# Kernel tuning notes

Measured on AMD Instinct MI355X. Metric: run time of the kernel, lower is better.

Reference implementation:

```python
import jax, jax.numpy as jnp
import numpy as np

EPS = 1e-6

def _layernorm(x, g, b):
    m = jnp.mean(x, axis=-1, keepdims=True)
    v = jnp.var(x, axis=-1, keepdims=True)
    return (x - m) / jnp.sqrt(v + EPS) * g + b

def setup_inputs() -> dict:
    key = jax.random.key(0)
    ks = jax.random.split(key, 12)
    B, L, D, H = 2, 1024, 1024, 16
    s = 0.02  # weight init scale
    return {
        "query": jax.random.normal(ks[0], (B, L, D), jnp.float32),
        "pos_bias": jax.random.normal(ks[1], (H, L, L), jnp.float32) * 0.1,
        "postag_bias": jax.random.normal(ks[2], (B, H, L, L), jnp.float32) * 0.1,
        "lex_mask": jax.random.normal(ks[3], (B, L), jnp.float32) * 0.1,
        "mask": jax.random.randint(ks[4], (B, L), 0, 2).astype(jnp.int32),
        "Wq": jax.random.normal(ks[5], (D, D), jnp.float32) * s,
        "bq": jnp.zeros((D,), jnp.float32),
        "Wk": jax.random.normal(ks[6], (D, D), jnp.float32) * s,
        "bk": jnp.zeros((D,), jnp.float32),
        "Wv": jax.random.normal(ks[7], (D, D), jnp.float32) * s,
        "bv": jnp.zeros((D,), jnp.float32),
        "Wo": jax.random.normal(ks[8], (D, D), jnp.float32) * s,
        "bo": jnp.zeros((D,), jnp.float32),
        "gamma": jnp.ones((D,), jnp.float32),
        "beta": jnp.zeros((D,), jnp.float32),
    }

def reference(query, pos_bias, postag_bias, lex_mask, mask,
              Wq, bq, Wk, bk, Wv, bv, Wo, bo, gamma, beta):
    B, L, D = query.shape
    H = pos_bias.shape[0]
    dk = D // H
    scale = jnp.asarray(dk ** 0.5, query.dtype)

    residual = query
    context = query              # context=None path: set BEFORE pre-LN norm
    qn = _layernorm(query, gamma, beta)  # pre_ln=True applies only to query

    Q = (qn @ Wq.T + bq).reshape(B, L, H, dk)       # bqhd
    K = (context @ Wk.T + bk).reshape(B, L, H, dk)  # bkhd
    V = (context @ Wv.T + bv).reshape(B, L, H, dk)

    # (B,H,L,S) logits with all additive bias terms
    logits = jnp.einsum('bqhd,bkhd->bhqk', Q, K) / scale
    logits = logits + pos_bias[None]               # rel-pos bias (H,L,S)
    logits = logits + postag_bias                  # POS-tag bias (B,H,L,S)
    logits = logits + lex_mask[:, None, None, :]   # additive lexical mask
    logits = jnp.where(mask[:, None, None, :] == 0, -jnp.inf, logits)

    attn = jax.nn.softmax(logits, axis=-1)         # dropout inactive (eval)
    out = jnp.einsum('bhqk,bkhd->bqhd', attn, V).reshape(B, L, D)
    out = out @ Wo.T + bo
    out = out + residual
    return out, attn
```

## Files before the change

kernel.cpp:

```cpp
#include <hip/hip_runtime.h>
#include <hip/hip_bf16.h>
#include <math.h>

constexpr int B = 2, L = 1024, D = 1024, H = 16, DK = 64;
constexpr int M = B * L;
constexpr int DD = D * D;

typedef __attribute__((ext_vector_type(8))) short bf16x8;
typedef __attribute__((ext_vector_type(4))) float f32x4;

__device__ inline unsigned short f2bf(float f) {
    __hip_bfloat16 h = __float2bfloat16(f);
    return __builtin_bit_cast(unsigned short, h);
}

__device__ inline void glds16(const void* g, void* l) {
    __builtin_amdgcn_global_load_lds((const __attribute__((address_space(1))) void*)g,
                                     (__attribute__((address_space(3))) void*)l,
                                     16, 0, 0);
}

__global__ __launch_bounds__(256) void ln2_kernel(const float* __restrict__ x,
                                                  const float* __restrict__ gamma,
                                                  const float* __restrict__ beta,
                                                  const float* __restrict__ lex,
                                                  const int* __restrict__ mask,
                                                  unsigned short* __restrict__ qn16,
                                                  unsigned short* __restrict__ q16,
                                                  float* __restrict__ lsmout) {
    int row = blockIdx.x;
    int t = threadIdx.x;
    if (t == 0) lsmout[row] = mask[row] ? lex[row] : -1e30f;
    const float4 v = ((const float4*)(x + (size_t)row * D))[t];
    float s  = v.x + v.y + v.z + v.w;
    float sq = v.x*v.x + v.y*v.y + v.z*v.z + v.w*v.w;
    #pragma unroll
    for (int m = 32; m >= 1; m >>= 1) {
        s  += __shfl_xor(s, m, 64);
        sq += __shfl_xor(sq, m, 64);
    }
    __shared__ float rs[4], rq[4];
    int wid = t >> 6;
    if ((t & 63) == 0) { rs[wid] = s; rq[wid] = sq; }
    __syncthreads();
    s  = rs[0] + rs[1] + rs[2] + rs[3];
    sq = rq[0] + rq[1] + rq[2] + rq[3];
    float mean = s * (1.0f / D);
    float var  = sq * (1.0f / D) - mean * mean;
    float rstd = rsqrtf(var + 1e-6f);
    float4 g  = ((const float4*)gamma)[t];
    float4 bb = ((const float4*)beta)[t];
    ushort4 on, oq;
    on.x = f2bf((v.x - mean) * rstd * g.x + bb.x);
    on.y = f2bf((v.y - mean) * rstd * g.y + bb.y);
    on.z = f2bf((v.z - mean) * rstd * g.z + bb.z);
    on.w = f2bf((v.w - mean) * rstd * g.w + bb.w);
    oq.x = f2bf(v.x); oq.y = f2bf(v.y); oq.z = f2bf(v.z); oq.w = f2bf(v.w);
    ((ushort4*)(qn16 + (size_t)row * D))[t] = on;
    ((ushort4*)(q16  + (size_t)row * D))[t] = oq;
}

__global__ __launch_bounds__(256) void wconv_kernel(const float* __restrict__ Wq,
                                                    const float* __restrict__ Wk,
                                                    const float* __restrict__ Wv,
                                                    const float* __restrict__ Wo,
                                                    unsigned short* __restrict__ out) {
    const float* src = (blockIdx.y == 0) ? Wq : (blockIdx.y == 1) ? Wk
                       : (blockIdx.y == 2) ? Wv : Wo;
    size_t i = (size_t)blockIdx.x * 256 + threadIdx.x;
    float4 v = ((const float4*)src)[i];
    ushort4 o;
    o.x = f2bf(v.x); o.y = f2bf(v.y); o.z = f2bf(v.z); o.w = f2bf(v.w);
    ((ushort4*)(out + (size_t)blockIdx.y * DD))[i] = o;
}

__global__ __launch_bounds__(256) void gemm_qkv(
        const unsigned short* __restrict__ qn16, const unsigned short* __restrict__ q16,
        const unsigned short* __restrict__ W,
        const float* __restrict__ bq, const float* __restrict__ bk,
        const float* __restrict__ bv,
        unsigned short* __restrict__ Qm, unsigned short* __restrict__ Km,
        unsigned short* __restrict__ Vm) {
    __shared__ __align__(16) unsigned short As[128 * 64];
    __shared__ __align__(16) unsigned short Ws[128 * 64];
    int t = threadIdx.x, lane = t & 63, w = t >> 6;
    int quad = lane >> 4, l15 = lane & 15;
    int nt = blockIdx.x;
    int bm = blockIdx.y * 128;
    const unsigned short* A = (nt < 8) ? qn16 : q16;
    const float* bias = (nt < 8) ? bq : ((nt < 16) ? bk : bv);
    unsigned short* Cout = (nt < 8) ? Qm : ((nt < 16) ? Km : Vm);
    int bn_local = (nt & 7) * 128;
    int wm = (w >> 1) * 64, wn = (w & 1) * 64;
    f32x4 acc[4][4] = {};
    for (int k0 = 0; k0 < D; k0 += 64) {
        __syncthreads();
        const unsigned short* ap = A + (size_t)(bm + w * 32) * D + k0;
        const unsigned short* wp = W + (size_t)(nt * 128 + w * 32) * D + k0;
        #pragma unroll
        for (int i = 0; i < 4; i++) {
            int c = i * 64 + lane;
            int r = c >> 3, g = (c & 7) ^ (r & 7);
            glds16(ap + (size_t)r * D + g * 8, &As[w * 2048 + i * 512]);
            glds16(wp + (size_t)r * D + g * 8, &Ws[w * 2048 + i * 512]);
        }
        __syncthreads();
        #pragma unroll
        for (int k2 = 0; k2 < 2; k2++) {
            bf16x8 av[4], bw[4];
            #pragma unroll
            for (int i = 0; i < 4; i++) {
                int r = wm + i * 16 + l15;
                av[i] = *(const bf16x8*)&As[r * 64 + (((quad + 4 * k2) ^ (r & 7)) * 8)];
            }
            #pragma unroll
            for (int j = 0; j < 4; j++) {
                int r = wn + j * 16 + l15;
                bw[j] = *(const bf16x8*)&Ws[r * 64 + (((quad + 4 * k2) ^ (r & 7)) * 8)];
            }
            #pragma unroll
            for (int i = 0; i < 4; i++)
                #pragma unroll
                for (int j = 0; j < 4; j++)
                    acc[i][j] = __builtin_amdgcn_mfma_f32_16x16x32_bf16(av[i], bw[j], acc[i][j], 0, 0, 0);
        }
    }
    #pragma unroll
    for (int j = 0; j < 4; j++) {
        int col = bn_local + wn + j * 16 + l15;
        float bcol = bias[col];
        #pragma unroll
        for (int i = 0; i < 4; i++)
            #pragma unroll
            for (int rg = 0; rg < 4; rg++) {
                int row = bm + wm + i * 16 + quad * 4 + rg;
                Cout[(size_t)row * D + col] = f2bf(acc[i][j][rg] + bcol);
            }
    }
}

__global__ __launch_bounds__(256) void vtrans_kernel(const unsigned short* __restrict__ Vm,
                                                     unsigned short* __restrict__ Vt) {
    __shared__ unsigned short sb[128 * 66];
    int t = threadIdx.x;
    int z = blockIdx.y;
    int b = z >> 4, h = z & 15;
    int s0 = blockIdx.x * 128;
    size_t base = (size_t)b * L * D + (size_t)h * 64;
    #pragma unroll
    for (int i = 0; i < 4; i++) {
        int idx = t + 256 * i;
        int r = idx >> 3, c8 = idx & 7;
        uint4 vv = *(const uint4*)&Vm[base + (size_t)(s0 + r) * D + c8 * 8];
        unsigned int* sp = (unsigned int*)&sb[r * 66 + c8 * 8];
        sp[0] = vv.x; sp[1] = vv.y; sp[2] = vv.z; sp[3] = vv.w;
    }
    __syncthreads();
    #pragma unroll
    for (int i = 0; i < 4; i++) {
        int idx = t + 256 * i;
        int d = idx >> 4, sc = idx & 15;
        unsigned short tmp[8];
        #pragma unroll
        for (int j = 0; j < 8; j++) tmp[j] = sb[(sc * 8 + j) * 66 + d];
        *(uint4*)&Vt[((size_t)z * 64 + d) * L + s0 + sc * 8] = *(uint4*)tmp;
    }
}

__global__ __launch_bounds__(256, 3) void attn_pv_kernel(
        const unsigned short* __restrict__ Qm, const unsigned short* __restrict__ Km,
        const unsigned short* __restrict__ Vt,
        const float* __restrict__ pos_bias, const float* __restrict__ postag,
        const float* __restrict__ lsm, float* __restrict__ attn_out,
        unsigned short* __restrict__ ctx16) {
    __shared__ __align__(16) unsigned short q_sh[16][72];
    __shared__ __align__(16) unsigned short p_sh[2][16][136];
    __shared__ float lsm_sh[1024];
    __shared__ float redA[16][4], redB[16][4];

    int t = threadIdx.x, lane = t & 63, w = t >> 6;
    int quad = lane >> 4, l15 = lane & 15;
    int qt = blockIdx.x & 63;
    int bh = blockIdx.x >> 6;
    int b = bh >> 4, h = bh & 15;
    int q0 = qt * 16;
    int q = q0 + l15;
    size_t base = (size_t)b * L * D + (size_t)h * DK;

    if (t < 128) {
        int r = t >> 3, c8 = t & 7;
        *(uint4*)&q_sh[r][c8 * 8] = *(const uint4*)&Qm[base + (size_t)(q0 + r) * D + c8 * 8];
    }
    ((float4*)lsm_sh)[t] = ((const float4*)(lsm + b * L))[t];
    __syncthreads();
    bf16x8 qb0 = *(const bf16x8*)&q_sh[l15][quad * 8];
    bf16x8 qb1 = *(const bf16x8*)&q_sh[l15][32 + quad * 8];

    const float* pbp = pos_bias + ((size_t)h * L + q) * L;
    const float* ptp = postag + ((size_t)bh * L + q) * L;
    const unsigned short* kp0 = Km + base + (size_t)((w) * 16 + l15) * D + quad * 8;
    const unsigned short* kp1 = Km + base + (size_t)((4 + w) * 16 + l15) * D + quad * 8;

    f32x4 acc[16] = {};
    #pragma unroll
    for (int st = 0; st < 8; st++) {
        size_t ko = (size_t)st * 128 * D;
        bf16x8 ka00 = *(const bf16x8*)(kp0 + ko);
        bf16x8 ka01 = *(const bf16x8*)(kp0 + ko + 32);
        bf16x8 ka10 = *(const bf16x8*)(kp1 + ko);
        bf16x8 ka11 = *(const bf16x8*)(kp1 + ko + 32);
        int s_u0 = st * 128 + w * 16 + quad * 4;
        int s_u1 = s_u0 + 64;
        float4 pb0 = *(const float4*)(pbp + s_u0);
        float4 pt0 = *(const float4*)(ptp + s_u0);
        float4 pb1 = *(const float4*)(pbp + s_u1);
        float4 pt1 = *(const float4*)(ptp + s_u1);
        float4 l0 = *(const float4*)&lsm_sh[s_u0];
        float4 l1 = *(const float4*)&lsm_sh[s_u1];
        int ti0 = 2 * st, ti1 = 2 * st + 1;
        acc[ti0] = __builtin_amdgcn_mfma_f32_16x16x32_bf16(ka00, qb0, acc[ti0], 0, 0, 0);
        acc[ti0] = __builtin_amdgcn_mfma_f32_16x16x32_bf16(ka01, qb1, acc[ti0], 0, 0, 0);
        acc[ti1] = __builtin_amdgcn_mfma_f32_16x16x32_bf16(ka10, qb0, acc[ti1], 0, 0, 0);
        acc[ti1] = __builtin_amdgcn_mfma_f32_16x16x32_bf16(ka11, qb1, acc[ti1], 0, 0, 0);
        acc[ti0][0] = acc[ti0][0] * 0.125f + (pb0.x + pt0.x + l0.x);
        acc[ti0][1] = acc[ti0][1] * 0.125f + (pb0.y + pt0.y + l0.y);
        acc[ti0][2] = acc[ti0][2] * 0.125f + (pb0.z + pt0.z + l0.z);
        acc[ti0][3] = acc[ti0][3] * 0.125f + (pb0.w + pt0.w + l0.w);
        acc[ti1][0] = acc[ti1][0] * 0.125f + (pb1.x + pt1.x + l1.x);
        acc[ti1][1] = acc[ti1][1] * 0.125f + (pb1.y + pt1.y + l1.y);
        acc[ti1][2] = acc[ti1][2] * 0.125f + (pb1.z + pt1.z + l1.z);
        acc[ti1][3] = acc[ti1][3] * 0.125f + (pb1.w + pt1.w + l1.w);
    }
    float mx = -1e30f;
    #pragma unroll
    for (int ti = 0; ti < 16; ti++)
        #pragma unroll
        for (int rg = 0; rg < 4; rg++) mx = fmaxf(mx, acc[ti][rg]);
    mx = fmaxf(mx, __shfl_xor(mx, 16, 64));
    mx = fmaxf(mx, __shfl_xor(mx, 32, 64));
    if (quad == 0) redA[l15][w] = mx;
    __syncthreads();
    mx = fmaxf(fmaxf(redA[l15][0], redA[l15][1]), fmaxf(redA[l15][2], redA[l15][3]));
    float sum = 0.f;
    #pragma unroll
    for (int ti = 0; ti < 16; ti++)
        #pragma unroll
        for (int rg = 0; rg < 4; rg++) {
            float e = __expf(acc[ti][rg] - mx);
            acc[ti][rg] = e;
            sum += e;
        }
    sum += __shfl_xor(sum, 16, 64);
    sum += __shfl_xor(sum, 32, 64);
    if (quad == 0) redB[l15][w] = sum;
    __syncthreads();
    float inv = 1.0f / (redB[l15][0] + redB[l15][1] + redB[l15][2] + redB[l15][3]);
    #pragma unroll
    for (int ti = 0; ti < 16; ti++) {
        int s0 = (ti >> 1) * 128 + (ti & 1) * 64 + w * 16 + quad * 4;
        float4 o;
        o.x = acc[ti][0] * inv; o.y = acc[ti][1] * inv;
        o.z = acc[ti][2] * inv; o.w = acc[ti][3] * inv;
        acc[ti][0] = o.x; acc[ti][1] = o.y; acc[ti][2] = o.z; acc[ti][3] = o.w;
        *(float4*)&attn_out[((size_t)bh * L + q) * L + s0] = o;
    }
    const unsigned short* vpl = Vt + ((size_t)bh * 64 + w * 16 + l15) * L + quad * 8;
    f32x4 cacc = {};
    bf16x8 vcur[4];
    #pragma unroll
    for (int kk = 0; kk < 4; kk++)
        vcur[kk] = *(const bf16x8*)(vpl + kk * 32);
    #pragma unroll
    for (int st = 0; st < 8; st++) {
        #pragma unroll
        for (int u = 0; u < 2; u++) {
            f32x4 p = acc[2 * st + u];
            ushort4 pu;
            pu.x = f2bf(p[0]); pu.y = f2bf(p[1]); pu.z = f2bf(p[2]); pu.w = f2bf(p[3]);
            *(ushort4*)&p_sh[st & 1][l15][u * 64 + w * 16 + quad * 4] = pu;
        }
        bf16x8 vnext[4];
        if (st < 7) {
            #pragma unroll
            for (int kk = 0; kk < 4; kk++)
                vnext[kk] = *(const bf16x8*)(vpl + (st + 1) * 128 + kk * 32);
        }
        asm volatile("s_waitcnt lgkmcnt(0)" ::: "memory");
        __builtin_amdgcn_sched_barrier(0);
        __builtin_amdgcn_s_barrier();
        __builtin_amdgcn_sched_barrier(0);
        #pragma unroll
        for (int kk = 0; kk < 4; kk++) {
            bf16x8 pf = *(const bf16x8*)&p_sh[st & 1][l15][kk * 32 + quad * 8];
            cacc = __builtin_amdgcn_mfma_f32_16x16x32_bf16(pf, vcur[kk], cacc, 0, 0, 0);
        }
        if (st < 7) {
            #pragma unroll
            for (int kk = 0; kk < 4; kk++) vcur[kk] = vnext[kk];
        }
    }
    size_t cbase = ((size_t)b * L + q0) * D + (size_t)h * 64 + w * 16 + l15;
    #pragma unroll
    for (int rg = 0; rg < 4; rg++)
        ctx16[cbase + (size_t)(quad * 4 + rg) * D] = f2bf(cacc[rg]);
}

__global__ __launch_bounds__(256) void gemm_out(
        const unsigned short* __restrict__ A, const unsigned short* __restrict__ W,
        const float* __restrict__ bias, const float* __restrict__ res,
        float* __restrict__ C) {
    __shared__ __align__(16) unsigned short As[64 * 64];
    __shared__ __align__(16) unsigned short Ws[64 * 64];
    int t = threadIdx.x, lane = t & 63, w = t >> 6;
    int quad = lane >> 4, l15 = lane & 15;
    int bm = blockIdx.x * 64, bn = blockIdx.y * 64;
    int wm = (w >> 1) * 32, wn = (w & 1) * 32;
    f32x4 acc[2][2] = {};
    for (int k0 = 0; k0 < D; k0 += 64) {
        __syncthreads();
        const unsigned short* ap = A + (size_t)(bm + w * 16) * D + k0;
        const unsigned short* wp = W + (size_t)(bn + w * 16) * D + k0;
        #pragma unroll
        for (int i = 0; i < 2; i++) {
            int c = i * 64 + lane;
            int r = c >> 3, g = (c & 7) ^ (r & 7);
            glds16(ap + (size_t)r * D + g * 8, &As[w * 1024 + i * 512]);
            glds16(wp + (size_t)r * D + g * 8, &Ws[w * 1024 + i * 512]);
        }
        __syncthreads();
        #pragma unroll
        for (int k2 = 0; k2 < 2; k2++) {
            bf16x8 av[2], bw[2];
            #pragma unroll
            for (int i = 0; i < 2; i++) {
                int r = wm + i * 16 + l15;
                av[i] = *(const bf16x8*)&As[r * 64 + (((quad + 4 * k2) ^ (r & 7)) * 8)];
            }
            #pragma unroll
            for (int j = 0; j < 2; j++) {
                int r = wn + j * 16 + l15;
                bw[j] = *(const bf16x8*)&Ws[r * 64 + (((quad + 4 * k2) ^ (r & 7)) * 8)];
            }
            #pragma unroll
            for (int i = 0; i < 2; i++)
                #pragma unroll
                for (int j = 0; j < 2; j++)
                    acc[i][j] = __builtin_amdgcn_mfma_f32_16x16x32_bf16(av[i], bw[j], acc[i][j], 0, 0, 0);
        }
    }
    #pragma unroll
    for (int j = 0; j < 2; j++) {
        int col = bn + wn + j * 16 + l15;
        float bcol = bias[col];
        #pragma unroll
        for (int i = 0; i < 2; i++)
            #pragma unroll
            for (int rg = 0; rg < 4; rg++) {
                int row = bm + wm + i * 16 + quad * 4 + rg;
                C[(size_t)row * D + col] = acc[i][j][rg] + bcol + res[(size_t)row * D + col];
            }
    }
}

extern "C" void kernel_launch(void* const* d_in, const int* in_sizes, int n_in,
                              void* d_out, int out_size, void* d_ws, size_t ws_size,
                              hipStream_t stream) {
    (void)in_sizes; (void)n_in; (void)out_size; (void)ws_size;
    const float* query  = (const float*)d_in[0];
    const float* pos_b  = (const float*)d_in[1];
    const float* postag = (const float*)d_in[2];
    const float* lex    = (const float*)d_in[3];
    const int*   mask   = (const int*)d_in[4];
    const float* Wq = (const float*)d_in[5];
    const float* bq = (const float*)d_in[6];
    const float* Wk = (const float*)d_in[7];
    const float* bk = (const float*)d_in[8];
    const float* Wv = (const float*)d_in[9];
    const float* bv = (const float*)d_in[10];
    const float* Wo = (const float*)d_in[11];
    const float* bo = (const float*)d_in[12];
    const float* gamma = (const float*)d_in[13];
    const float* beta  = (const float*)d_in[14];

    float* out  = (float*)d_out;
    float* attn = out + (size_t)B * L * D;

    unsigned short* ws16 = (unsigned short*)d_ws;
    const size_t NE = (size_t)M * D;
    unsigned short* qn16  = ws16;
    unsigned short* q16   = ws16 + NE;
    unsigned short* W16   = ws16 + 2 * NE;
    unsigned short* Qm16  = W16 + 4 * (size_t)DD;
    unsigned short* Km16  = Qm16 + NE;
    unsigned short* Vm16  = Km16 + NE;
    unsigned short* Vt16  = Vm16 + NE;
    unsigned short* ctx16 = Vt16 + NE;
    float* lsm = (float*)(ctx16 + NE);

    ln2_kernel<<<M, 256, 0, stream>>>(query, gamma, beta, lex, mask, qn16, q16, lsm);
    wconv_kernel<<<dim3(DD / 1024, 4), 256, 0, stream>>>(Wq, Wk, Wv, Wo, W16);
    gemm_qkv<<<dim3(24, 16), 256, 0, stream>>>(qn16, q16, W16, bq, bk, bv,
                                               Qm16, Km16, Vm16);
    vtrans_kernel<<<dim3(8, 32), 256, 0, stream>>>(Vm16, Vt16);
    attn_pv_kernel<<<B * H * (L / 16), 256, 0, stream>>>(Qm16, Km16, Vt16,
                                                         pos_b, postag, lsm,
                                                         attn, ctx16);
    gemm_out<<<dim3(32, 16), 256, 0, stream>>>(ctx16, W16 + 3 * (size_t)DD, bo, query, out);
}
```

Baseline: 432.1 us.

## Stage K, bias and V tiles through swizzled LDS with async global_load_lds double-buffering

```diff
diff --git a/kernel.cpp b/kernel.cpp
--- a/kernel.cpp
+++ b/kernel.cpp
@@ -8,6 +8,8 @@
 
 typedef __attribute__((ext_vector_type(8))) short bf16x8;
 typedef __attribute__((ext_vector_type(4))) float f32x4;
+
+#define SB0() __builtin_amdgcn_sched_barrier(0)
 
 __device__ inline unsigned short f2bf(float f) {
     __hip_bfloat16 h = __float2bfloat16(f);
@@ -167,14 +169,15 @@
     }
 }
 
-__global__ __launch_bounds__(256, 3) void attn_pv_kernel(
+__global__ __launch_bounds__(256, 2) void attn_pv_kernel(
         const unsigned short* __restrict__ Qm, const unsigned short* __restrict__ Km,
         const unsigned short* __restrict__ Vt,
         const float* __restrict__ pos_bias, const float* __restrict__ postag,
         const float* __restrict__ lsm, float* __restrict__ attn_out,
         unsigned short* __restrict__ ctx16) {
+    __shared__ __align__(16) unsigned short pool[32768];
+    __shared__ __align__(16) unsigned short p_sh[16][136];
     __shared__ __align__(16) unsigned short q_sh[16][72];
-    __shared__ __align__(16) unsigned short p_sh[2][16][136];
     __shared__ float lsm_sh[1024];
     __shared__ float redA[16][4], redB[16][4];
 
@@ -196,28 +199,80 @@
     bf16x8 qb0 = *(const bf16x8*)&q_sh[l15][quad * 8];
     bf16x8 qb1 = *(const bf16x8*)&q_sh[l15][32 + quad * 8];
 
-    const float* pbp = pos_bias + ((size_t)h * L + q) * L;
-    const float* ptp = postag + ((size_t)bh * L + q) * L;
-    const unsigned short* kp0 = Km + base + (size_t)((w) * 16 + l15) * D + quad * 8;
-    const unsigned short* kp1 = Km + base + (size_t)((4 + w) * 16 + l15) * D + quad * 8;
+    const float* pbQ = pos_bias + ((size_t)h * L + q0) * L;
+    const float* ptQ = postag + ((size_t)bh * L + q0) * L;
 
     f32x4 acc[16] = {};
+    SB0();
+    {
+        const unsigned short* kpn = Km + base + (size_t)(w * 32) * D;
+        #pragma unroll
+        for (int i = 0; i < 4; i++) {
+            int r = i * 8 + (lane >> 3);
+            int g = (lane & 7) ^ (r & 7);
+            glds16(kpn + (size_t)r * D + g * 8, &pool[w * 2048 + i * 512]);
+        }
+    }
+    SB0();
+    {
+        int rb = lane >> 3;
+        int gb = (lane & 7) ^ rb;
+        #pragma unroll
+        for (int i = 0; i < 2; i++) {
+            glds16(pbQ + (size_t)(i * 8 + rb) * L + w * 32 + gb * 4,
+                   &pool[16384 + w * 2048 + i * 512]);
+            glds16(ptQ + (size_t)(i * 8 + rb) * L + w * 32 + gb * 4,
+                   &pool[16384 + w * 2048 + 1024 + i * 512]);
+        }
+    }
+    SB0();
     #pragma unroll
     for (int st = 0; st < 8; st++) {
-        size_t ko = (size_t)st * 128 * D;
-        bf16x8 ka00 = *(const bf16x8*)(kp0 + ko);
-        bf16x8 ka01 = *(const bf16x8*)(kp0 + ko + 32);
-        bf16x8 ka10 = *(const bf16x8*)(kp1 + ko);
-        bf16x8 ka11 = *(const bf16x8*)(kp1 + ko + 32);
-        int s_u0 = st * 128 + w * 16 + quad * 4;
-        int s_u1 = s_u0 + 64;
-        float4 pb0 = *(const float4*)(pbp + s_u0);
-        float4 pt0 = *(const float4*)(ptp + s_u0);
-        float4 pb1 = *(const float4*)(pbp + s_u1);
-        float4 pt1 = *(const float4*)(ptp + s_u1);
+        int bc = st & 1, bn = bc ^ 1;
+        if (st < 7) {
+            SB0();
+            const unsigned short* kpn = Km + base + (size_t)((st + 1) * 128 + w * 32) * D;
+            #pragma unroll
+            for (int i = 0; i < 4; i++) {
+                int r = i * 8 + (lane >> 3);
+                int g = (lane & 7) ^ (r & 7);
+                glds16(kpn + (size_t)r * D + g * 8, &pool[bn * 8192 + w * 2048 + i * 512]);
+            }
+            SB0();
+            {
+                int rb = lane >> 3;
+                int gb = (lane & 7) ^ rb;
+                #pragma unroll
+                for (int i = 0; i < 2; i++) {
+                    glds16(pbQ + (size_t)(i * 8 + rb) * L + (st + 1) * 128 + w * 32 + gb * 4,
+                           &pool[16384 + bn * 8192 + w * 2048 + i * 512]);
+                    glds16(ptQ + (size_t)(i * 8 + rb) * L + (st + 1) * 128 + w * 32 + gb * 4,
+                           &pool[16384 + bn * 8192 + w * 2048 + 1024 + i * 512]);
+                }
+            }
+            SB0();
+            asm volatile("s_waitcnt vmcnt(8)" ::: "memory");
+        } else {
+            SB0();
+            asm volatile("s_waitcnt vmcnt(0)" ::: "memory");
+        }
+        SB0();
+        int r7 = l15 & 7;
+        const unsigned short* kB = &pool[bc * 8192 + w * 2048];
+        bf16x8 ka00 = *(const bf16x8*)&kB[l15 * 64 + ((quad ^ r7) * 8)];
+        bf16x8 ka01 = *(const bf16x8*)&kB[l15 * 64 + (((quad + 4) ^ r7) * 8)];
+        bf16x8 ka10 = *(const bf16x8*)&kB[(16 + l15) * 64 + ((quad ^ r7) * 8)];
+        bf16x8 ka11 = *(const bf16x8*)&kB[(16 + l15) * 64 + (((quad + 4) ^ r7) * 8)];
+        const float* pbL = (const float*)&pool[16384 + bc * 8192 + w * 2048];
+        const float* ptL = (const float*)&pool[16384 + bc * 8192 + w * 2048 + 1024];
+        float4 pb0 = *(const float4*)&pbL[l15 * 32 + ((quad ^ r7) * 4)];
+        float4 pb1 = *(const float4*)&pbL[l15 * 32 + (((quad + 4) ^ r7) * 4)];
+        float4 pt0 = *(const float4*)&ptL[l15 * 32 + ((quad ^ r7) * 4)];
+        float4 pt1 = *(const float4*)&ptL[l15 * 32 + (((quad + 4) ^ r7) * 4)];
+        int s_u0 = st * 128 + w * 32 + quad * 4;
         float4 l0 = *(const float4*)&lsm_sh[s_u0];
-        float4 l1 = *(const float4*)&lsm_sh[s_u1];
-        int ti0 = 2 * st, ti1 = 2 * st + 1;
+        float4 l1 = *(const float4*)&lsm_sh[s_u0 + 16];
+        int ti0 = 2 * st, ti1 = ti0 + 1;
         acc[ti0] = __builtin_amdgcn_mfma_f32_16x16x32_bf16(ka00, qb0, acc[ti0], 0, 0, 0);
         acc[ti0] = __builtin_amdgcn_mfma_f32_16x16x32_bf16(ka01, qb1, acc[ti0], 0, 0, 0);
         acc[ti1] = __builtin_amdgcn_mfma_f32_16x16x32_bf16(ka10, qb0, acc[ti1], 0, 0, 0);
@@ -257,47 +312,62 @@
     float inv = 1.0f / (redB[l15][0] + redB[l15][1] + redB[l15][2] + redB[l15][3]);
     #pragma unroll
     for (int ti = 0; ti < 16; ti++) {
-        int s0 = (ti >> 1) * 128 + (ti & 1) * 64 + w * 16 + quad * 4;
+        int s0 = (ti >> 1) * 128 + w * 32 + (ti & 1) * 16 + quad * 4;
         float4 o;
         o.x = acc[ti][0] * inv; o.y = acc[ti][1] * inv;
         o.z = acc[ti][2] * inv; o.w = acc[ti][3] * inv;
         acc[ti][0] = o.x; acc[ti][1] = o.y; acc[ti][2] = o.z; acc[ti][3] = o.w;
         *(float4*)&attn_out[((size_t)bh * L + q) * L + s0] = o;
     }
-    const unsigned short* vpl = Vt + ((size_t)bh * 64 + w * 16 + l15) * L + quad * 8;
     f32x4 cacc = {};
-    bf16x8 vcur[4];
-    #pragma unroll
-    for (int kk = 0; kk < 4; kk++)
-        vcur[kk] = *(const bf16x8*)(vpl + kk * 32);
+    const unsigned short* vbase = Vt + ((size_t)bh * 64 + w * 16) * L;
+    SB0();
+    #pragma unroll
+    for (int i = 0; i < 4; i++) {
+        int r = i * 4 + (lane >> 4);
+        int g = (lane & 15) ^ (r & 7);
+        glds16(vbase + (size_t)r * L + g * 8, &pool[w * 2048 + i * 512]);
+    }
+    SB0();
     #pragma unroll
     for (int st = 0; st < 8; st++) {
+        int bc = st & 1;
         #pragma unroll
         for (int u = 0; u < 2; u++) {
             f32x4 p = acc[2 * st + u];
             ushort4 pu;
             pu.x = f2bf(p[0]); pu.y = f2bf(p[1]); pu.z = f2bf(p[2]); pu.w = f2bf(p[3]);
-            *(ushort4*)&p_sh[st & 1][l15][u * 64 + w * 16 + quad * 4] = pu;
-        }
-        bf16x8 vnext[4];
+            *(ushort4*)&p_sh[l15][w * 32 + u * 16 + quad * 4] = pu;
+        }
         if (st < 7) {
-            #pragma unroll
-            for (int kk = 0; kk < 4; kk++)
-                vnext[kk] = *(const bf16x8*)(vpl + (st + 1) * 128 + kk * 32);
+            SB0();
+            #pragma unroll
+            for (int i = 0; i < 4; i++) {
+                int r = i * 4 + (lane >> 4);
+                int g = (lane & 15) ^ (r & 7);
+                glds16(vbase + (size_t)r * L + (st + 1) * 128 + g * 8,
+                       &pool[(bc ^ 1) * 8192 + w * 2048 + i * 512]);
+            }
+            SB0();
+            asm volatile("s_waitcnt vmcnt(4)" ::: "memory");
+        } else {
+            SB0();
+            asm volatile("s_waitcnt vmcnt(0)" ::: "memory");
         }
         asm volatile("s_waitcnt lgkmcnt(0)" ::: "memory");
-        __builtin_amdgcn_sched_barrier(0);
+        SB0();
         __builtin_amdgcn_s_barrier();
-        __builtin_amdgcn_sched_barrier(0);
+        SB0();
+        const unsigned short* vB = &pool[bc * 8192 + w * 2048];
         #pragma unroll
         for (int kk = 0; kk < 4; kk++) {
-            bf16x8 pf = *(const bf16x8*)&p_sh[st & 1][l15][kk * 32 + quad * 8];
-            cacc = __builtin_amdgcn_mfma_f32_16x16x32_bf16(pf, vcur[kk], cacc, 0, 0, 0);
-        }
-        if (st < 7) {
-            #pragma unroll
-            for (int kk = 0; kk < 4; kk++) vcur[kk] = vnext[kk];
-        }
+            bf16x8 vf = *(const bf16x8*)&vB[l15 * 128 + (((kk * 4 + quad) ^ (l15 & 7)) * 8)];
+            bf16x8 pf = *(const bf16x8*)&p_sh[l15][kk * 32 + quad * 8];
+            cacc = __builtin_amdgcn_mfma_f32_16x16x32_bf16(pf, vf, cacc, 0, 0, 0);
+        }
+        SB0();
+        __builtin_amdgcn_s_barrier();
+        SB0();
     }
     size_t cbase = ((size_t)b * L + q0) * D + (size_t)h * 64 + w * 16 + l15;
     #pragma unroll
```

Result: faster. 402.2 us (-6.9%).
